# Performance work log

Measured on AMD Instinct MI355X. Metric: run time of the kernel, lower is better.

Reference implementation:

```python
import jax, jax.numpy as jnp
import numpy as np

B, L, D, C = 1, 512, 128, 128  # batch, length, input_dim, channel_dim


def _layernorm(x, w, b, eps=1e-5):
    mu = jnp.mean(x, axis=-1, keepdims=True)
    var = jnp.var(x, axis=-1, keepdims=True)
    return (x - mu) * jax.lax.rsqrt(var + eps) * w + b


def setup_inputs() -> dict:
    key = jax.random.key(0)
    ks = jax.random.split(key, 12)
    s = 0.05  # weight scale ~ xavier for d=128
    f32 = jnp.float32
    return {
        "z": jax.random.normal(ks[0], (B, L, L, D), f32),
        "ln_in_w": jnp.ones((D,), f32), "ln_in_b": jnp.zeros((D,), f32),
        "Wga": jax.random.normal(ks[1], (D, C), f32) * s, "bga": jnp.zeros((C,), f32),
        "Wla": jax.random.normal(ks[2], (D, C), f32) * s, "bla": jnp.zeros((C,), f32),
        "Wgb": jax.random.normal(ks[3], (D, C), f32) * s, "bgb": jnp.zeros((C,), f32),
        "Wlb": jax.random.normal(ks[4], (D, C), f32) * s, "blb": jnp.zeros((C,), f32),
        "ln_o_w": jnp.ones((C,), f32), "ln_o_b": jnp.zeros((C,), f32),
        "Wgo": jax.random.normal(ks[5], (D, D), f32) * s, "bgo": jnp.zeros((D,), f32),
        "Wlo": jax.random.normal(ks[6], (C, D), f32) * s, "blo": jnp.zeros((D,), f32),
    }


def reference(z, ln_in_w, ln_in_b, Wga, bga, Wla, bla, Wgb, bgb, Wlb, blb,
              ln_o_w, ln_o_b, Wgo, bgo, Wlo, blo):
    # z: [B, L, L, D]
    zn = _layernorm(z, ln_in_w, ln_in_b)
    a = jax.nn.sigmoid(zn @ Wga + bga) * (zn @ Wla + bla)   # [B,L,L,C]
    b = jax.nn.sigmoid(zn @ Wgb + bgb) * (zn @ Wlb + blb)   # [B,L,L,C]
    # triangular update (axis=1): per-channel L x L matmul
    # k[b,i,j,c] = sum_m a[b,i,m,c] * b[b,m,j,c]
    k = jnp.einsum('bimc,bmjc->bijc', a, b)
    out = jax.nn.sigmoid(zn @ Wgo + bgo) * (_layernorm(k, ln_o_w, ln_o_b) @ Wlo + blo)
    return out
```

## Files before the change

### kernel.cpp

```cpp
#include <hip/hip_runtime.h>

typedef unsigned short u16;
typedef __attribute__((ext_vector_type(8))) short bf16x8;
typedef __attribute__((ext_vector_type(4))) float f32x4;

#define L_ 512
#define D_ 128
#define LL_ (512*512)
#define LP_ 136
#define TP_ 72

#define WT_OFF 0
#define AT_OFF 98304
#define BT_OFF (AT_OFF + 128*LL_)
#define KT_OFF (BT_OFF + 128*LL_)

union U16x8 { uint4 u4; bf16x8 v; u16 s[8]; };

__device__ __forceinline__ u16 f2bf(float f){
  union { float f; unsigned int i; } w; w.f = f;
  unsigned int r = w.i + 0x7FFFu + ((w.i >> 16) & 1u);
  return (u16)(r >> 16);
}
__device__ __forceinline__ float sigm(float x){
  return 1.0f / (1.0f + __expf(-x));
}

__global__ __launch_bounds__(256) void conv_kernel(
    const float* __restrict__ Wga, const float* __restrict__ Wla,
    const float* __restrict__ Wgb, const float* __restrict__ Wlb,
    const float* __restrict__ Wgo, const float* __restrict__ Wlo,
    u16* __restrict__ wt)
{
  int idx = blockIdx.x*256 + threadIdx.x;
  int w = idx >> 14, rem = idx & 16383, n = rem >> 7, k = rem & 127;
  const float* src;
  switch (w){
    case 0: src = Wga; break; case 1: src = Wla; break; case 2: src = Wgb; break;
    case 3: src = Wlb; break; case 4: src = Wgo; break; default: src = Wlo;
  }
  wt[idx] = f2bf(src[k*128 + n]);
}

__device__ __forceinline__ void gemm128(const u16* znlds, const u16* __restrict__ wtm,
                                        int wm, int wn, int quad, int l16, f32x4 acc[4][4])
{
  bf16x8 bf[4][4];
#pragma unroll
  for (int nt = 0; nt < 4; ++nt){
    int n = wn*64 + nt*16 + l16;
#pragma unroll
    for (int kc = 0; kc < 4; ++kc){
      U16x8 u; u.u4 = *(const uint4*)(wtm + n*128 + kc*32 + quad*8);
      bf[nt][kc] = u.v;
    }
  }
#pragma unroll
  for (int mt = 0; mt < 4; ++mt){
    int row = wm*64 + mt*16 + l16;
    bf16x8 af[4];
#pragma unroll
    for (int kc = 0; kc < 4; ++kc)
      af[kc] = *(const bf16x8*)(znlds + row*LP_ + kc*32 + quad*8);
#pragma unroll
    for (int nt = 0; nt < 4; ++nt)
#pragma unroll
      for (int kc = 0; kc < 4; ++kc)
        acc[mt][nt] = __builtin_amdgcn_mfma_f32_16x16x32_bf16(af[kc], bf[nt][kc], acc[mt][nt], 0, 0, 0);
  }
}

__device__ __forceinline__ void gemm64(const u16* alds, const u16* __restrict__ wtm,
                                       int wm, int wn, int quad, int l16, f32x4 acc[2][4])
{
  bf16x8 bf[4][4];
#pragma unroll
  for (int nt = 0; nt < 4; ++nt){
    int n = wn*64 + nt*16 + l16;
#pragma unroll
    for (int kc = 0; kc < 4; ++kc){
      U16x8 u; u.u4 = *(const uint4*)(wtm + n*128 + kc*32 + quad*8);
      bf[nt][kc] = u.v;
    }
  }
#pragma unroll
  for (int mt = 0; mt < 2; ++mt){
    int row = wm*32 + mt*16 + l16;
    bf16x8 af[4];
#pragma unroll
    for (int kc = 0; kc < 4; ++kc)
      af[kc] = *(const bf16x8*)(alds + row*LP_ + kc*32 + quad*8);
#pragma unroll
    for (int nt = 0; nt < 4; ++nt)
#pragma unroll
      for (int kc = 0; kc < 4; ++kc)
        acc[mt][nt] = __builtin_amdgcn_mfma_f32_16x16x32_bf16(af[kc], bf[nt][kc], acc[mt][nt], 0, 0, 0);
  }
}

__global__ __launch_bounds__(256) void stageA_kernel(
    const float* __restrict__ z, const float* __restrict__ lnw, const float* __restrict__ lnb,
    const u16* __restrict__ wt,
    const float* __restrict__ bga, const float* __restrict__ bla,
    const float* __restrict__ bgb, const float* __restrict__ blb,
    u16* __restrict__ a_t, u16* __restrict__ b_tt)
{
  __shared__ __align__(16) u16 zn[128*LP_];
  __shared__ __align__(16) u16 trh[9216];

  const int bid = blockIdx.x;
  const int type = bid >> 11;
  const int tile = bid & 2047;
  const int outer = tile >> 2;
  const int seg = tile & 3;

  const int t = threadIdx.x;
  const int r = t >> 1, h = t & 1;
  const int lane = t & 63, wave = t >> 6;
  const int quad = lane >> 4, l16 = lane & 15;
  const int wm = wave & 1, wn = wave >> 1;

  {
    int gpos = (type == 0) ? (outer*L_ + seg*128 + r) : ((seg*128 + r)*L_ + outer);
    const float* zrow = z + gpos*D_ + h*64;
    float raw[64];
    float sum = 0.f, sq = 0.f;
#pragma unroll
    for (int q = 0; q < 16; ++q){
      float4 v = *(const float4*)(zrow + q*4);
      raw[q*4+0] = v.x; raw[q*4+1] = v.y; raw[q*4+2] = v.z; raw[q*4+3] = v.w;
      sum += v.x + v.y + v.z + v.w;
      sq  += v.x*v.x + v.y*v.y + v.z*v.z + v.w*v.w;
    }
    sum += __shfl_xor(sum, 1, 64);
    sq  += __shfl_xor(sq , 1, 64);
    float mu = sum * (1.f/128.f);
    float rstd = rsqrtf(sq*(1.f/128.f) - mu*mu + 1e-5f);
#pragma unroll
    for (int q = 0; q < 8; ++q){
      U16x8 o;
#pragma unroll
      for (int e = 0; e < 8; ++e){
        int d = h*64 + q*8 + e;
        o.s[e] = f2bf((raw[q*8+e] - mu)*rstd*lnw[d] + lnb[d]);
      }
      *(uint4*)(zn + r*LP_ + h*64 + q*8) = o.u4;
    }
  }
  __syncthreads();

  const u16* wg   = wt + (type ? 2 : 0)*16384;
  const u16* wl   = wt + (type ? 3 : 1)*16384;
  const float* bgp = type ? bgb : bga;
  const float* blp = type ? blb : bla;
  const f32x4 z4 = {0.f, 0.f, 0.f, 0.f};

  f32x4 accG[4][4], accL[4][4];
#pragma unroll
  for (int mt = 0; mt < 4; ++mt)
#pragma unroll
    for (int nt = 0; nt < 4; ++nt){ accG[mt][nt] = z4; accL[mt][nt] = z4; }

  gemm128(zn, wg, wm, wn, quad, l16, accG);
#pragma unroll
  for (int nt = 0; nt < 4; ++nt){
    float bb = bgp[wn*64 + nt*16 + l16];
#pragma unroll
    for (int mt = 0; mt < 4; ++mt)
#pragma unroll
      for (int e = 0; e < 4; ++e)
        accG[mt][nt][e] = sigm(accG[mt][nt][e] + bb);
  }
  gemm128(zn, wl, wm, wn, quad, l16, accL);
#pragma unroll
  for (int nt = 0; nt < 4; ++nt){
    float bb = blp[wn*64 + nt*16 + l16];
#pragma unroll
    for (int mt = 0; mt < 4; ++mt)
#pragma unroll
      for (int e = 0; e < 4; ++e)
        accG[mt][nt][e] *= (accL[mt][nt][e] + bb);
  }

  u16* dst = type ? b_tt : a_t;
  const int base = outer*L_ + seg*128;
#pragma unroll
  for (int pass = 0; pass < 2; ++pass){
    if (wm == pass){
#pragma unroll
      for (int nt = 0; nt < 4; ++nt){
        int gcol = wn*64 + nt*16 + l16;
#pragma unroll
        for (int mt = 0; mt < 4; ++mt)
#pragma unroll
          for (int e = 0; e < 4; ++e)
            trh[gcol*TP_ + mt*16 + quad*4 + e] = f2bf(accG[mt][nt][e]);
      }
    }
    __syncthreads();
#pragma unroll
    for (int q = 0; q < 4; ++q){
      uint4 v = *(const uint4*)(trh + r*TP_ + h*32 + q*8);
      *(uint4*)(dst + r*LL_ + base + pass*64 + h*32 + q*8) = v;
    }
    __syncthreads();
  }
}

__global__ __launch_bounds__(256) void stageT_kernel(
    const u16* __restrict__ a_t, const u16* __restrict__ b_tt, u16* __restrict__ k_t)
{
  __shared__ __align__(16) u16 As[2][128*64];
  __shared__ __align__(16) u16 Bs[2][128*64];
  const int c = blockIdx.y;
  const int it = blockIdx.x >> 2, jt = blockIdx.x & 3;
  const u16* Ab = a_t + c*LL_ + it*128*L_;
  const u16* Bb = b_tt + c*LL_ + jt*128*L_;
  const int t = threadIdx.x;
  const int lane = t & 63, wave = t >> 6;
  const int quad = lane >> 4, l16 = lane & 15;
  const int wm = wave & 1, wn = wave >> 1;
  const int sr8 = lane >> 3, scl = lane & 7;
  const int cgx = scl ^ sr8;
  const int swz = (l16 & 7) << 3;

  f32x4 acc[4][4];
  const f32x4 z4 = {0.f,0.f,0.f,0.f};
#pragma unroll
  for (int mt = 0; mt < 4; ++mt)
#pragma unroll
    for (int nt = 0; nt < 4; ++nt) acc[mt][nt] = z4;

  auto stage = [&](int b, int k0){
#pragma unroll
    for (int q = 0; q < 4; ++q){
      int row = q*32 + wave*8 + sr8;
      __builtin_amdgcn_global_load_lds(
          (const __attribute__((address_space(1))) void*)(Ab + row*L_ + k0 + cgx*8),
          (__attribute__((address_space(3))) void*)(&As[b][(q*32 + wave*8)*64]),
          16, 0, 0);
    }
#pragma unroll
    for (int q = 0; q < 4; ++q){
      int row = q*32 + wave*8 + sr8;
      __builtin_amdgcn_global_load_lds(
          (const __attribute__((address_space(1))) void*)(Bb + row*L_ + k0 + cgx*8),
          (__attribute__((address_space(3))) void*)(&Bs[b][(q*32 + wave*8)*64]),
          16, 0, 0);
    }
  };

  stage(0, 0);
  for (int kt = 0; kt < 8; ++kt){
    const int cur = kt & 1;
    if (kt < 7){
      stage(cur ^ 1, (kt + 1)*64);
      asm volatile("s_waitcnt vmcnt(8)" ::: "memory");
    } else {
      asm volatile("s_waitcnt vmcnt(0)" ::: "memory");
    }
    __builtin_amdgcn_s_barrier();
    asm volatile("" ::: "memory");
    const u16* Ac = &As[cur][0];
    const u16* Bc = &Bs[cur][0];
    bf16x8 bfr[4][2];
#pragma unroll
    for (int nt = 0; nt < 4; ++nt){
      int brow = wn*64 + nt*16 + l16;
#pragma unroll
      for (int ks = 0; ks < 2; ++ks)
        bfr[nt][ks] = *(const bf16x8*)(Bc + brow*64 + (((ks*4 + quad)*8) ^ swz));
    }
#pragma unroll
    for (int mt = 0; mt < 4; ++mt){
      int arow = wm*64 + mt*16 + l16;
      bf16x8 af[2];
#pragma unroll
      for (int ks = 0; ks < 2; ++ks)
        af[ks] = *(const bf16x8*)(Ac + arow*64 + (((ks*4 + quad)*8) ^ swz));
#pragma unroll
      for (int nt = 0; nt < 4; ++nt)
#pragma unroll
        for (int ks = 0; ks < 2; ++ks)
          acc[mt][nt] = __builtin_amdgcn_mfma_f32_16x16x32_bf16(af[ks], bfr[nt][ks], acc[mt][nt], 0, 0, 0);
    }
    asm volatile("" ::: "memory");
    __builtin_amdgcn_s_barrier();
    asm volatile("" ::: "memory");
  }

#pragma unroll
  for (int mt = 0; mt < 4; ++mt)
#pragma unroll
    for (int nt = 0; nt < 4; ++nt){
      int gcol = wn*64 + nt*16 + l16;
#pragma unroll
      for (int e = 0; e < 4; ++e){
        int grow = wm*64 + mt*16 + quad*4 + e;
        k_t[c*LL_ + (it*128 + grow)*L_ + jt*128 + gcol] = f2bf(acc[mt][nt][e]);
      }
    }
}

__global__ __launch_bounds__(256) void stageC_kernel(
    const u16* __restrict__ k_t, const float* __restrict__ z,
    const u16* __restrict__ wt,
    const float* __restrict__ lnw, const float* __restrict__ lnb,
    const float* __restrict__ onw, const float* __restrict__ onb,
    const float* __restrict__ bgo, const float* __restrict__ blo,
    float* __restrict__ out)
{
  __shared__ __align__(16) u16 kl[128*TP_];
  __shared__ __align__(16) u16 zn2[64*LP_];
  __shared__ __align__(16) u16 znp[64*LP_];
  const u16* wtgo = wt + 4*16384;
  const u16* wtlo = wt + 5*16384;
  const int bx = blockIdx.x;
  const int pos0 = (bx >> 3)*L_ + (bx & 7)*64;
  const int t = threadIdx.x, r = t >> 1, h = t & 1;
  const int rl4 = t >> 2, qd = t & 3;
  const int lane = t & 63, wave = t >> 6;
  const int quad = lane >> 4, l16 = lane & 15;
  const int wm = wave & 1, wn = wave >> 1;

#pragma unroll
  for (int q = 0; q < 4; ++q)
    *(uint4*)(kl + r*TP_ + h*32 + q*8) = *(const uint4*)(k_t + r*LL_ + pos0 + h*32 + q*8);
  __syncthreads();

  {
    float sum = 0.f, sq = 0.f;
    float kv[32];
#pragma unroll
    for (int q = 0; q < 32; ++q){
      union { unsigned int i; float f; } w;
      w.i = ((unsigned int)kl[(qd*32 + q)*TP_ + rl4]) << 16;
      kv[q] = w.f; sum += w.f; sq += w.f*w.f;
    }
    sum += __shfl_xor(sum, 1, 64); sq += __shfl_xor(sq, 1, 64);
    sum += __shfl_xor(sum, 2, 64); sq += __shfl_xor(sq, 2, 64);
    float mu = sum*(1.f/128.f);
    float rstd = rsqrtf(sq*(1.f/128.f) - mu*mu + 1e-5f);
#pragma unroll
    for (int q = 0; q < 4; ++q){
      U16x8 o;
#pragma unroll
      for (int e = 0; e < 8; ++e){
        int cch = qd*32 + q*8 + e;
        o.s[e] = f2bf((kv[q*8+e] - mu)*rstd*onw[cch] + onb[cch]);
      }
      *(uint4*)(zn2 + rl4*LP_ + qd*32 + q*8) = o.u4;
    }
  }
  {
    const float* zr = z + (pos0 + rl4)*D_ + qd*32;
    float zv[32];
    float sum = 0.f, sq = 0.f;
#pragma unroll
    for (int q = 0; q < 8; ++q){
      float4 v = *(const float4*)(zr + q*4);
      zv[q*4+0] = v.x; zv[q*4+1] = v.y; zv[q*4+2] = v.z; zv[q*4+3] = v.w;
      sum += v.x + v.y + v.z + v.w;
      sq  += v.x*v.x + v.y*v.y + v.z*v.z + v.w*v.w;
    }
    sum += __shfl_xor(sum, 1, 64); sq += __shfl_xor(sq, 1, 64);
    sum += __shfl_xor(sum, 2, 64); sq += __shfl_xor(sq, 2, 64);
    float mu = sum*(1.f/128.f);
    float rstd = rsqrtf(sq*(1.f/128.f) - mu*mu + 1e-5f);
#pragma unroll
    for (int q = 0; q < 4; ++q){
      U16x8 o;
#pragma unroll
      for (int e = 0; e < 8; ++e){
        int cch = qd*32 + q*8 + e;
        o.s[e] = f2bf((zv[q*8+e] - mu)*rstd*lnw[cch] + lnb[cch]);
      }
      *(uint4*)(znp + rl4*LP_ + qd*32 + q*8) = o.u4;
    }
  }
  __syncthreads();

  f32x4 accK[2][4], accO[2][4];
  const f32x4 z4 = {0.f,0.f,0.f,0.f};
#pragma unroll
  for (int mt = 0; mt < 2; ++mt)
#pragma unroll
    for (int nt = 0; nt < 4; ++nt){ accK[mt][nt] = z4; accO[mt][nt] = z4; }

  gemm64(zn2, wtlo, wm, wn, quad, l16, accK);
  gemm64(znp, wtgo, wm, wn, quad, l16, accO);

#pragma unroll
  for (int nt = 0; nt < 4; ++nt){
    int gcol = wn*64 + nt*16 + l16;
    float bo = bgo[gcol], bl = blo[gcol];
#pragma unroll
    for (int mt = 0; mt < 2; ++mt)
#pragma unroll
      for (int e = 0; e < 4; ++e){
        int grow = wm*32 + mt*16 + quad*4 + e;
        float s = sigm(accO[mt][nt][e] + bo);
        out[(pos0 + grow)*D_ + gcol] = s*(accK[mt][nt][e] + bl);
      }
  }
}

extern "C" void kernel_launch(void* const* d_in, const int* in_sizes, int n_in,
                              void* d_out, int out_size, void* d_ws, size_t ws_size,
                              hipStream_t stream)
{
  const float* z   = (const float*)d_in[0];
  const float* lnw = (const float*)d_in[1];
  const float* lnb = (const float*)d_in[2];
  const float* Wga = (const float*)d_in[3];
  const float* bga = (const float*)d_in[4];
  const float* Wla = (const float*)d_in[5];
  const float* bla = (const float*)d_in[6];
  const float* Wgb = (const float*)d_in[7];
  const float* bgb = (const float*)d_in[8];
  const float* Wlb = (const float*)d_in[9];
  const float* blb = (const float*)d_in[10];
  const float* onw = (const float*)d_in[11];
  const float* onb = (const float*)d_in[12];
  const float* Wgo = (const float*)d_in[13];
  const float* bgo = (const float*)d_in[14];
  const float* Wlo = (const float*)d_in[15];
  const float* blo = (const float*)d_in[16];

  u16* ws   = (u16*)d_ws;
  u16* wt   = ws + WT_OFF;
  u16* a_t  = ws + AT_OFF;
  u16* b_tt = ws + BT_OFF;
  u16* k_t  = ws + KT_OFF;
  float* out = (float*)d_out;

  conv_kernel<<<384, 256, 0, stream>>>(Wga, Wla, Wgb, Wlb, Wgo, Wlo, wt);
  stageA_kernel<<<4096, 256, 0, stream>>>(z, lnw, lnb, wt, bga, bla, bgb, blb, a_t, b_tt);
  stageT_kernel<<<dim3(16, 128), 256, 0, stream>>>(a_t, b_tt, k_t);
  stageC_kernel<<<4096, 256, 0, stream>>>(k_t, z, wt, lnw, lnb, onw, onb, bgo, blo, out);
}
```

Measured before the change: 635.5 us.

## Fold layernorm affine into weights, shrink LDS, single-buffer stageT with swizzled block order

After: 826.5 us. 30.1% more time.

```diff
diff --git a/kernel.cpp b/kernel.cpp
--- a/kernel.cpp
+++ b/kernel.cpp
@@ -11,11 +11,13 @@
 #define TP_ 72
 
 #define WT_OFF 0
-#define AT_OFF 98304
+#define B2_OFF 98304
+#define AT_OFF (B2_OFF + 1536)
 #define BT_OFF (AT_OFF + 128*LL_)
 #define KT_OFF (BT_OFF + 128*LL_)
 
 union U16x8 { uint4 u4; bf16x8 v; u16 s[8]; };
+union U16x4 { ushort4 v; u16 s[4]; };
 
 __device__ __forceinline__ u16 f2bf(float f){
   union { float f; unsigned int i; } w; w.f = f;
@@ -30,16 +32,37 @@
     const float* __restrict__ Wga, const float* __restrict__ Wla,
     const float* __restrict__ Wgb, const float* __restrict__ Wlb,
     const float* __restrict__ Wgo, const float* __restrict__ Wlo,
-    u16* __restrict__ wt)
-{
-  int idx = blockIdx.x*256 + threadIdx.x;
-  int w = idx >> 14, rem = idx & 16383, n = rem >> 7, k = rem & 127;
-  const float* src;
-  switch (w){
-    case 0: src = Wga; break; case 1: src = Wla; break; case 2: src = Wgb; break;
-    case 3: src = Wlb; break; case 4: src = Wgo; break; default: src = Wlo;
-  }
-  wt[idx] = f2bf(src[k*128 + n]);
+    const float* __restrict__ lnw, const float* __restrict__ lnb,
+    const float* __restrict__ onw, const float* __restrict__ onb,
+    const float* __restrict__ bga, const float* __restrict__ bla,
+    const float* __restrict__ bgb, const float* __restrict__ blb,
+    const float* __restrict__ bgo, const float* __restrict__ blo,
+    u16* __restrict__ wt, float* __restrict__ bias2)
+{
+  if (blockIdx.x < 384){
+    int idx = blockIdx.x*256 + threadIdx.x;
+    int w = idx >> 14, rem = idx & 16383, n = rem >> 7, k = rem & 127;
+    const float* src;
+    switch (w){
+      case 0: src = Wga; break; case 1: src = Wla; break; case 2: src = Wgb; break;
+      case 3: src = Wlb; break; case 4: src = Wgo; break; default: src = Wlo;
+    }
+    float sc = (w == 5) ? onw[k] : lnw[k];
+    wt[idx] = f2bf(src[k*128 + n] * sc);
+  } else {
+    int j = (blockIdx.x - 384)*256 + threadIdx.x;
+    int w = j >> 7, n = j & 127;
+    const float* src; const float* bs;
+    switch (w){
+      case 0: src = Wga; bs = bga; break; case 1: src = Wla; bs = bla; break;
+      case 2: src = Wgb; bs = bgb; break; case 3: src = Wlb; bs = blb; break;
+      case 4: src = Wgo; bs = bgo; break; default: src = Wlo; bs = blo;
+    }
+    const float* lb = (w == 5) ? onb : lnb;
+    float acc = bs[n];
+    for (int k = 0; k < 128; ++k) acc += lb[k] * src[k*128 + n];
+    bias2[j] = acc;
+  }
 }
 
 __device__ __forceinline__ void gemm128(const u16* znlds, const u16* __restrict__ wtm,
@@ -98,15 +121,14 @@
   }
 }
 
-__global__ __launch_bounds__(256) void stageA_kernel(
-    const float* __restrict__ z, const float* __restrict__ lnw, const float* __restrict__ lnb,
-    const u16* __restrict__ wt,
-    const float* __restrict__ bga, const float* __restrict__ bla,
-    const float* __restrict__ bgb, const float* __restrict__ blb,
+__global__ __launch_bounds__(256, 4) void stageA_kernel(
+    const float* __restrict__ z, const u16* __restrict__ wt,
+    const float* __restrict__ bias2,
     u16* __restrict__ a_t, u16* __restrict__ b_tt)
 {
-  __shared__ __align__(16) u16 zn[128*LP_];
-  __shared__ __align__(16) u16 trh[9216];
+  __shared__ __align__(16) u16 smem[128*LP_];
+  u16* zn = smem;
+  u16* trh = smem;
 
   const int bid = blockIdx.x;
   const int type = bid >> 11;
@@ -140,10 +162,8 @@
     for (int q = 0; q < 8; ++q){
       U16x8 o;
 #pragma unroll
-      for (int e = 0; e < 8; ++e){
-        int d = h*64 + q*8 + e;
-        o.s[e] = f2bf((raw[q*8+e] - mu)*rstd*lnw[d] + lnb[d]);
-      }
+      for (int e = 0; e < 8; ++e)
+        o.s[e] = f2bf((raw[q*8+e] - mu)*rstd);
       *(uint4*)(zn + r*LP_ + h*64 + q*8) = o.u4;
     }
   }
@@ -151,8 +171,8 @@
 
   const u16* wg   = wt + (type ? 2 : 0)*16384;
   const u16* wl   = wt + (type ? 3 : 1)*16384;
-  const float* bgp = type ? bgb : bga;
-  const float* blp = type ? blb : bla;
+  const float* bgp = bias2 + (type ? 2 : 0)*128;
+  const float* blp = bias2 + (type ? 3 : 1)*128;
   const f32x4 z4 = {0.f, 0.f, 0.f, 0.f};
 
   f32x4 accG[4][4], accL[4][4];
@@ -182,6 +202,8 @@
         accG[mt][nt][e] *= (accL[mt][nt][e] + bb);
   }
 
+  __syncthreads();
+
   u16* dst = type ? b_tt : a_t;
   const int base = outer*L_ + seg*128;
 #pragma unroll
@@ -191,10 +213,13 @@
       for (int nt = 0; nt < 4; ++nt){
         int gcol = wn*64 + nt*16 + l16;
 #pragma unroll
-        for (int mt = 0; mt < 4; ++mt)
+        for (int mt = 0; mt < 4; ++mt){
+          U16x4 pk;
 #pragma unroll
           for (int e = 0; e < 4; ++e)
-            trh[gcol*TP_ + mt*16 + quad*4 + e] = f2bf(accG[mt][nt][e]);
+            pk.s[e] = f2bf(accG[mt][nt][e]);
+          *(ushort4*)(trh + gcol*TP_ + mt*16 + quad*4) = pk.v;
+        }
       }
     }
     __syncthreads();
@@ -207,13 +232,14 @@
   }
 }
 
-__global__ __launch_bounds__(256) void stageT_kernel(
+__global__ __launch_bounds__(256, 4) void stageT_kernel(
     const u16* __restrict__ a_t, const u16* __restrict__ b_tt, u16* __restrict__ k_t)
 {
-  __shared__ __align__(16) u16 As[2][128*64];
-  __shared__ __align__(16) u16 Bs[2][128*64];
-  const int c = blockIdx.y;
-  const int it = blockIdx.x >> 2, jt = blockIdx.x & 3;
+  __shared__ __align__(16) u16 As[128*64];
+  __shared__ __align__(16) u16 Bs[128*64];
+  const int bid = blockIdx.x;
+  const int lid = (bid & 7)*256 + (bid >> 3);
+  const int c = lid >> 4, it = (lid >> 2) & 3, jt = lid & 3;
   const u16* Ab = a_t + c*LL_ + it*128*L_;
   const u16* Bb = b_tt + c*LL_ + jt*128*L_;
   const int t = threadIdx.x;
@@ -231,13 +257,14 @@
 #pragma unroll
     for (int nt = 0; nt < 4; ++nt) acc[mt][nt] = z4;
 
-  auto stage = [&](int b, int k0){
+  for (int kt = 0; kt < 8; ++kt){
+    const int k0 = kt*64;
 #pragma unroll
     for (int q = 0; q < 4; ++q){
       int row = q*32 + wave*8 + sr8;
       __builtin_amdgcn_global_load_lds(
           (const __attribute__((address_space(1))) void*)(Ab + row*L_ + k0 + cgx*8),
-          (__attribute__((address_space(3))) void*)(&As[b][(q*32 + wave*8)*64]),
+          (__attribute__((address_space(3))) void*)(&As[(q*32 + wave*8)*64]),
           16, 0, 0);
     }
 #pragma unroll
@@ -245,31 +272,17 @@
       int row = q*32 + wave*8 + sr8;
       __builtin_amdgcn_global_load_lds(
           (const __attribute__((address_space(1))) void*)(Bb + row*L_ + k0 + cgx*8),
-          (__attribute__((address_space(3))) void*)(&Bs[b][(q*32 + wave*8)*64]),
+          (__attribute__((address_space(3))) void*)(&Bs[(q*32 + wave*8)*64]),
           16, 0, 0);
     }
-  };
-
-  stage(0, 0);
-  for (int kt = 0; kt < 8; ++kt){
-    const int cur = kt & 1;
-    if (kt < 7){
-      stage(cur ^ 1, (kt + 1)*64);
-      asm volatile("s_waitcnt vmcnt(8)" ::: "memory");
-    } else {
-      asm volatile("s_waitcnt vmcnt(0)" ::: "memory");
-    }
-    __builtin_amdgcn_s_barrier();
-    asm volatile("" ::: "memory");
-    const u16* Ac = &As[cur][0];
-    const u16* Bc = &Bs[cur][0];
+    __syncthreads();
     bf16x8 bfr[4][2];
 #pragma unroll
     for (int nt = 0; nt < 4; ++nt){
       int brow = wn*64 + nt*16 + l16;
 #pragma unroll
       for (int ks = 0; ks < 2; ++ks)
-        bfr[nt][ks] = *(const bf16x8*)(Bc + brow*64 + (((ks*4 + quad)*8) ^ swz));
+        bfr[nt][ks] = *(const bf16x8*)(Bs + brow*64 + (((ks*4 + quad)*8) ^ swz));
     }
 #pragma unroll
     for (int mt = 0; mt < 4; ++mt){
@@ -277,16 +290,14 @@
       bf16x8 af[2];
 #pragma unroll
       for (int ks = 0; ks < 2; ++ks)
-        af[ks] = *(const bf16x8*)(Ac + arow*64 + (((ks*4 + quad)*8) ^ swz));
+        af[ks] = *(const bf16x8*)(As + arow*64 + (((ks*4 + quad)*8) ^ swz));
 #pragma unroll
       for (int nt = 0; nt < 4; ++nt)
 #pragma unroll
         for (int ks = 0; ks < 2; ++ks)
           acc[mt][nt] = __builtin_amdgcn_mfma_f32_16x16x32_bf16(af[ks], bfr[nt][ks], acc[mt][nt], 0, 0, 0);
     }
-    asm volatile("" ::: "memory");
-    __builtin_amdgcn_s_barrier();
-    asm volatile("" ::: "memory");
+    __syncthreads();
   }
 
 #pragma unroll
@@ -302,19 +313,17 @@
     }
 }
 
-__global__ __launch_bounds__(256) void stageC_kernel(
+__global__ __launch_bounds__(256, 4) void stageC_kernel(
     const u16* __restrict__ k_t, const float* __restrict__ z,
-    const u16* __restrict__ wt,
-    const float* __restrict__ lnw, const float* __restrict__ lnb,
-    const float* __restrict__ onw, const float* __restrict__ onb,
-    const float* __restrict__ bgo, const float* __restrict__ blo,
+    const u16* __restrict__ wt, const float* __restrict__ bias2,
     float* __restrict__ out)
 {
-  __shared__ __align__(16) u16 kl[128*TP_];
   __shared__ __align__(16) u16 zn2[64*LP_];
-  __shared__ __align__(16) u16 znp[64*LP_];
+  __shared__ __align__(16) u16 kbuf[128*TP_];
   const u16* wtgo = wt + 4*16384;
   const u16* wtlo = wt + 5*16384;
+  const float* bgo2 = bias2 + 4*128;
+  const float* blo2 = bias2 + 5*128;
   const int bx = blockIdx.x;
   const int pos0 = (bx >> 3)*L_ + (bx & 7)*64;
   const int t = threadIdx.x, r = t >> 1, h = t & 1;
@@ -325,7 +334,7 @@
 
 #pragma unroll
   for (int q = 0; q < 4; ++q)
-    *(uint4*)(kl + r*TP_ + h*32 + q*8) = *(const uint4*)(k_t + r*LL_ + pos0 + h*32 + q*8);
+    *(uint4*)(kbuf + r*TP_ + h*32 + q*8) = *(const uint4*)(k_t + r*LL_ + pos0 + h*32 + q*8);
   __syncthreads();
 
   {
@@ -334,7 +343,7 @@
 #pragma unroll
     for (int q = 0; q < 32; ++q){
       union { unsigned int i; float f; } w;
-      w.i = ((unsigned int)kl[(qd*32 + q)*TP_ + rl4]) << 16;
+      w.i = ((unsigned int)kbuf[(qd*32 + q)*TP_ + rl4]) << 16;
       kv[q] = w.f; sum += w.f; sq += w.f*w.f;
     }
     sum += __shfl_xor(sum, 1, 64); sq += __shfl_xor(sq, 1, 64);
@@ -345,13 +354,13 @@
     for (int q = 0; q < 4; ++q){
       U16x8 o;
 #pragma unroll
-      for (int e = 0; e < 8; ++e){
-        int cch = qd*32 + q*8 + e;
-        o.s[e] = f2bf((kv[q*8+e] - mu)*rstd*onw[cch] + onb[cch]);
-      }
+      for (int e = 0; e < 8; ++e)
+        o.s[e] = f2bf((kv[q*8+e] - mu)*rstd);
       *(uint4*)(zn2 + rl4*LP_ + qd*32 + q*8) = o.u4;
     }
   }
+  __syncthreads();
+
   {
     const float* zr = z + (pos0 + rl4)*D_ + qd*32;
     float zv[32];
@@ -371,11 +380,9 @@
     for (int q = 0; q < 4; ++q){
       U16x8 o;
 #pragma unroll
-      for (int e = 0; e < 8; ++e){
-        int cch = qd*32 + q*8 + e;
-        o.s[e] = f2bf((zv[q*8+e] - mu)*rstd*lnw[cch] + lnb[cch]);
-      }
-      *(uint4*)(znp + rl4*LP_ + qd*32 + q*8) = o.u4;
+      for (int e = 0; e < 8; ++e)
+        o.s[e] = f2bf((zv[q*8+e] - mu)*rstd);
+      *(uint4*)(kbuf + rl4*LP_ + qd*32 + q*8) = o.u4;
     }
   }
   __syncthreads();
@@ -387,13 +394,13 @@
 #pragma unroll
     for (int nt = 0; nt < 4; ++nt){ accK[mt][nt] = z4; accO[mt][nt] = z4; }
 
-  gemm64(zn2, wtlo, wm, wn, quad, l16, accK);
-  gemm64(znp, wtgo, wm, wn, quad, l16, accO);
+  gemm64(zn2,  wtlo, wm, wn, quad, l16, accK);
+  gemm64(kbuf, wtgo, wm, wn, quad, l16, accO);
 
 #pragma unroll
   for (int nt = 0; nt < 4; ++nt){
     int gcol = wn*64 + nt*16 + l16;
-    float bo = bgo[gcol], bl = blo[gcol];
+    float bo = bgo2[gcol], bl = blo2[gcol];
 #pragma unroll
     for (int mt = 0; mt < 2; ++mt)
 #pragma unroll
@@ -429,13 +436,16 @@
 
   u16* ws   = (u16*)d_ws;
   u16* wt   = ws + WT_OFF;
+  float* b2 = (float*)(ws + B2_OFF);
   u16* a_t  = ws + AT_OFF;
   u16* b_tt = ws + BT_OFF;
   u16* k_t  = ws + KT_OFF;
   float* out = (float*)d_out;
 
-  conv_kernel<<<384, 256, 0, stream>>>(Wga, Wla, Wgb, Wlb, Wgo, Wlo, wt);
-  stageA_kernel<<<4096, 256, 0, stream>>>(z, lnw, lnb, wt, bga, bla, bgb, blb, a_t, b_tt);
-  stageT_kernel<<<dim3(16, 128), 256, 0, stream>>>(a_t, b_tt, k_t);
-  stageC_kernel<<<4096, 256, 0, stream>>>(k_t, z, wt, lnw, lnb, onw, onb, bgo, blo, out);
-}
+  conv_kernel<<<387, 256, 0, stream>>>(Wga, Wla, Wgb, Wlb, Wgo, Wlo,
+                                       lnw, lnb, onw, onb,
+                                       bga, bla, bgb, blb, bgo, blo, wt, b2);
+  stageA_kernel<<<4096, 256, 0, stream>>>(z, wt, b2, a_t, b_tt);
+  stageT_kernel<<<2048, 256, 0, stream>>>(a_t, b_tt, k_t);
+  stageC_kernel<<<4096, 256, 0, stream>>>(k_t, z, wt, b2, out);
+}
```
